# Optimization experiments

Measured on AMD Instinct MI355X. Metric: run time of the kernel, lower is better.

## Reference

```python
import jax, jax.numpy as jnp
import numpy as np

N_QUBITS = 10
N_LAYERS = 4
DIM = 2 ** N_QUBITS  # 1024
IN_FEATURES = 512
OUT_FEATURES = 64
BATCH = 4096


def setup_inputs() -> dict:
    key = jax.random.key(0)
    ks = jax.random.split(key, 6)
    return {
        "x": jax.random.normal(ks[0], (BATCH, IN_FEATURES), dtype=jnp.float32),
        "W_pre": jax.random.normal(ks[1], (DIM, IN_FEATURES), dtype=jnp.float32) / np.float32(np.sqrt(IN_FEATURES)),
        "b_pre": jnp.zeros((DIM,), dtype=jnp.float32),
        "q_weights": jax.random.normal(ks[2], (N_LAYERS, N_QUBITS, 3), dtype=jnp.float32),
        "W_post": jax.random.normal(ks[3], (OUT_FEATURES, N_QUBITS), dtype=jnp.float32) / np.float32(np.sqrt(N_QUBITS)),
        "b_post": jnp.zeros((OUT_FEATURES,), dtype=jnp.float32),
    }


def _rot_matrices(w):
    # w: [L, n, 3] -> PennyLane Rot(phi, theta, omega) = RZ(omega) RY(theta) RZ(phi)
    phi, theta, omega = w[..., 0], w[..., 1], w[..., 2]
    c = jnp.cos(theta / 2).astype(jnp.complex64)
    s = jnp.sin(theta / 2).astype(jnp.complex64)
    e_mm = jnp.exp(-0.5j * (phi + omega))
    e_pp = jnp.exp(0.5j * (phi + omega))
    e_pm = jnp.exp(0.5j * (phi - omega))
    e_mp = jnp.exp(-0.5j * (phi - omega))
    row0 = jnp.stack([e_mm * c, -e_pm * s], axis=-1)
    row1 = jnp.stack([e_mp * s, e_pp * c], axis=-1)
    return jnp.stack([row0, row1], axis=-2)  # [L, n, 2, 2] complex64


def _apply_1q(psi, U, wire):
    # psi: [B, 2, 2, ..., 2]; apply 2x2 unitary U on qubit `wire` (axis wire+1)
    axis = wire + 1
    psi = jnp.moveaxis(psi, axis, -1)
    psi = psi @ U.T  # new[a] = sum_b U[a,b] psi[b]
    return jnp.moveaxis(psi, -1, axis)


def _cnot(psi, control, target):
    ca, ta = control + 1, target + 1
    p0 = jax.lax.index_in_dim(psi, 0, ca, keepdims=True)
    p1 = jax.lax.index_in_dim(psi, 1, ca, keepdims=True)
    p1 = jnp.flip(p1, axis=ta)  # flip target amplitudes where control = 1
    return jnp.concatenate([p0, p1], axis=ca)


def _quantum_forward(amps, q_weights):
    # AmplitudeEmbedding(normalize=True) + StronglyEntanglingLayers + PauliZ expvals, batched.
    B = amps.shape[0]
    norm = jnp.sqrt(jnp.sum(amps * amps, axis=1, keepdims=True))
    psi = (amps / norm).astype(jnp.complex64).reshape((B,) + (2,) * N_QUBITS)
    U = _rot_matrices(q_weights)
    for l in range(N_LAYERS):
        for w in range(N_QUBITS):
            psi = _apply_1q(psi, U[l, w], w)
        r = (l % (N_QUBITS - 1)) + 1  # PennyLane default ranges
        for w in range(N_QUBITS):
            psi = _cnot(psi, w, (w + r) % N_QUBITS)
    probs = psi.real ** 2 + psi.imag ** 2
    axes_all = tuple(range(1, N_QUBITS + 1))
    z = []
    for i in range(N_QUBITS):
        other = tuple(a for a in axes_all if a != i + 1)
        marg = jnp.sum(probs, axis=other)  # [B, 2]
        z.append(marg[:, 0] - marg[:, 1])
    return jnp.stack(z, axis=1)  # [B, n_qubits]


def reference(x, W_pre, b_pre, q_weights, W_post, b_post):
    h = jax.nn.relu(x @ W_pre.T + b_pre)          # [B, 2^n]
    z = _quantum_forward(h, q_weights)            # [B, n_qubits]
    return z @ W_post.T + b_post                  # [B, out_features]
```

## Files before the change

kernel.cpp:

```cpp
#include <hip/hip_runtime.h>
#include <hip/hip_bf16.h>
#include <math.h>

#define NQ   10
#define DIM  1024
#define NL   4
#define INF  512
#define OUTF 64
#define MBATCH 4096

typedef _Float16 half8 __attribute__((ext_vector_type(8)));
typedef float f32x4 __attribute__((ext_vector_type(4)));

#define WS_H16  0
#define WS_X16  (8u * 1024u * 1024u)
#define WS_W16  (12u * 1024u * 1024u)
#define WS_SU   (13u * 1024u * 1024u)

__global__ __launch_bounds__(256) void setup_kernel(
    const float* __restrict__ x, const float* __restrict__ w,
    const float* __restrict__ qw, _Float16* __restrict__ x16,
    _Float16* __restrict__ w16, float* __restrict__ su)
{
    const int bid = blockIdx.x;
    const int tid = threadIdx.x;
    if (bid < 1024) {
        const int base = bid * 2048 + tid * 8;
        float4 a = *reinterpret_cast<const float4*>(x + base);
        float4 b = *reinterpret_cast<const float4*>(x + base + 4);
        half8 o = {(_Float16)a.x, (_Float16)a.y, (_Float16)a.z, (_Float16)a.w,
                   (_Float16)b.x, (_Float16)b.y, (_Float16)b.z, (_Float16)b.w};
        *reinterpret_cast<half8*>(x16 + base) = o;
    } else if (bid < 1280) {
        const int base = (bid - 1024) * 2048 + tid * 8;
        float4 a = *reinterpret_cast<const float4*>(w + base);
        float4 b = *reinterpret_cast<const float4*>(w + base + 4);
        half8 o = {(_Float16)a.x, (_Float16)a.y, (_Float16)a.z, (_Float16)a.w,
                   (_Float16)b.x, (_Float16)b.y, (_Float16)b.z, (_Float16)b.w};
        *reinterpret_cast<half8*>(w16 + base) = o;
    } else {
        if (tid < NL * NQ) {
            float phi = qw[tid * 3 + 0], theta = qw[tid * 3 + 1], omega = qw[tid * 3 + 2];
            float st, ct; sincosf(0.5f * theta, &st, &ct);
            float spm, cpm; sincosf(0.5f * (phi - omega), &spm, &cpm);
            float spp, cpp; sincosf(0.5f * (phi + omega), &spp, &cpp);
            float* o = su + tid * 8;
            o[0] =  cpp * ct; o[1] = -spp * ct;
            o[2] = -cpm * st; o[3] = -spm * st;
            o[4] =  cpm * st; o[5] = -spm * st;
            o[6] =  cpp * ct; o[7] =  spp * ct;
        }
    }
}

__global__ __launch_bounds__(256) void gemm16_kernel(
    const _Float16* __restrict__ X, const _Float16* __restrict__ W,
    const float* __restrict__ bias, _Float16* __restrict__ H)
{
    constexpr int BM = 128, BN = 64, BK = 32, LDP = BK + 8;
    __shared__ _Float16 As[BM][LDP];
    __shared__ _Float16 Bs[BN][LDP];

    const int tid = threadIdx.x;
    const int wave = tid >> 6, lane = tid & 63;
    const int wm = wave >> 1, wn = wave & 1;
    const int l15 = lane & 15, lk = (lane >> 4) * 8;

    const int arow = tid >> 1, ahalf = tid & 1;
    const int brow = tid & 63, bseg = tid >> 6;

    const _Float16* ag = X + (size_t)(blockIdx.x * BM + arow) * INF + ahalf * 16;
    const _Float16* bg = W + (size_t)(blockIdx.y * BN + brow) * INF + bseg * 8;

    f32x4 acc[4][2] = {};

    for (int k0 = 0; k0 < INF; k0 += BK) {
        half8 av0 = *reinterpret_cast<const half8*>(ag + k0);
        half8 av1 = *reinterpret_cast<const half8*>(ag + k0 + 8);
        half8 bv  = *reinterpret_cast<const half8*>(bg + k0);
        __syncthreads();
        *reinterpret_cast<half8*>(&As[arow][ahalf * 16])     = av0;
        *reinterpret_cast<half8*>(&As[arow][ahalf * 16 + 8]) = av1;
        *reinterpret_cast<half8*>(&Bs[brow][bseg * 8])       = bv;
        __syncthreads();
        half8 bfr0 = *reinterpret_cast<const half8*>(&Bs[wn * 32 + l15][lk]);
        half8 bfr1 = *reinterpret_cast<const half8*>(&Bs[wn * 32 + 16 + l15][lk]);
#pragma unroll
        for (int mi = 0; mi < 4; ++mi) {
            half8 afr = *reinterpret_cast<const half8*>(&As[wm * 64 + mi * 16 + l15][lk]);
            acc[mi][0] = __builtin_amdgcn_mfma_f32_16x16x32_f16(afr, bfr0, acc[mi][0], 0, 0, 0);
            acc[mi][1] = __builtin_amdgcn_mfma_f32_16x16x32_f16(afr, bfr1, acc[mi][1], 0, 0, 0);
        }
    }

    const int crow0 = blockIdx.x * BM + wm * 64;
    const int ccol0 = blockIdx.y * BN + wn * 32;
#pragma unroll
    for (int ni = 0; ni < 2; ++ni) {
        const int col = ccol0 + ni * 16 + l15;
        const float bb = bias[col];
#pragma unroll
        for (int mi = 0; mi < 4; ++mi) {
#pragma unroll
            for (int r = 0; r < 4; ++r) {
                const int row = crow0 + mi * 16 + (lane >> 4) * 4 + r;
                const float o = fmaxf(acc[mi][ni][r] + bb, 0.f);
                H[(size_t)row * DIM + col] = (_Float16)o;
            }
        }
    }
}

template<int ML>
__device__ __forceinline__ float lxor(float v, int bpa) {
    if constexpr (ML == 32)
        return __int_as_float(__builtin_amdgcn_ds_bpermute(bpa, __float_as_int(v)));
    else if constexpr (ML == 16)
        return __int_as_float(__builtin_amdgcn_ds_swizzle(__float_as_int(v), 0x401F));
    else if constexpr (ML == 8)
        return __int_as_float(__builtin_amdgcn_mov_dpp(__float_as_int(v), 0x128, 0xF, 0xF, false));
    else if constexpr (ML == 4)
        return __int_as_float(__builtin_amdgcn_ds_swizzle(__float_as_int(v), 0x101F));
    else if constexpr (ML == 2)
        return __int_as_float(__builtin_amdgcn_mov_dpp(__float_as_int(v), 0x4E, 0xF, 0xF, false));
    else
        return __int_as_float(__builtin_amdgcn_mov_dpp(__float_as_int(v), 0xB1, 0xF, 0xF, false));
}

__device__ __forceinline__ int perm_chain(int j, int r) {
#pragma unroll
    for (int w2 = NQ - 1; w2 >= 0; --w2) {
        const int cb = 9 - w2;
        const int tb = 9 - ((w2 + r) % NQ);
        j ^= ((j >> cb) & 1) << tb;
    }
    return j;
}

template<int W>
__device__ __forceinline__ void lane_gate(float re[16], float im[16],
                                          const float* up, int lane, int bpa) {
    constexpr int ML = 1 << (5 - W);
    const float4 ua = *reinterpret_cast<const float4*>(up + W * 8);
    const float4 ub = *reinterpret_cast<const float4*>(up + W * 8 + 4);
    const bool hi = (lane & ML) != 0;
    const float cmr = hi ? ub.z : ua.x;
    const float cmi = hi ? ub.w : ua.y;
    const float cpr = hi ? ub.x : ua.z;
    const float cpi = hi ? ub.y : ua.w;
#pragma unroll
    for (int k = 0; k < 16; ++k) {
        const float pr = lxor<ML>(re[k], bpa);
        const float pi = lxor<ML>(im[k], bpa);
        const float ar = re[k], ai = im[k];
        re[k] = cmr * ar - cmi * ai + cpr * pr - cpi * pi;
        im[k] = cmr * ai + cmi * ar + cpr * pi + cpi * pr;
    }
}

__global__ __launch_bounds__(64) void quantum_kernel(
    const _Float16* __restrict__ Hbuf, const float* __restrict__ sug,
    const float* __restrict__ W_post, const float* __restrict__ b_post,
    float* __restrict__ out)
{
    __shared__ float sre[DIM];
    __shared__ float sim[DIM];

    const int lane = threadIdx.x;
    const int b = blockIdx.x;
    const int bpa = (lane ^ 32) << 2;

    const _Float16* hr = Hbuf + (size_t)b * DIM + (lane << 4);
    float re[16], im[16];
    {
        half8 h0 = *reinterpret_cast<const half8*>(hr);
        half8 h1 = *reinterpret_cast<const half8*>(hr + 8);
#pragma unroll
        for (int j = 0; j < 8; ++j) { re[j] = (float)h0[j]; re[8 + j] = (float)h1[j]; }
    }
    float nrm = 0.f;
#pragma unroll
    for (int k = 0; k < 16; ++k) nrm = fmaf(re[k], re[k], nrm);
#pragma unroll
    for (int m = 1; m < 64; m <<= 1) nrm += __shfl_xor(nrm, m, 64);
    const float rn = rsqrtf(nrm);
#pragma unroll
    for (int k = 0; k < 16; ++k) { re[k] *= rn; im[k] = 0.f; }

    for (int l = 0; l < NL; ++l) {
        const float* up = sug + l * NQ * 8;

        lane_gate<0>(re, im, up, lane, bpa);
        lane_gate<1>(re, im, up, lane, bpa);
        lane_gate<2>(re, im, up, lane, bpa);
        lane_gate<3>(re, im, up, lane, bpa);
        lane_gate<4>(re, im, up, lane, bpa);
        lane_gate<5>(re, im, up, lane, bpa);

#pragma unroll
        for (int w = 6; w < 10; ++w) {
            const int mk = 1 << (9 - w);
            const float4 ua = *reinterpret_cast<const float4*>(up + w * 8);
            const float4 ub = *reinterpret_cast<const float4*>(up + w * 8 + 4);
#pragma unroll
            for (int k = 0; k < 16; ++k) {
                if (!(k & mk)) {
                    const int k1 = k | mk;
                    const float a0r = re[k], a0i = im[k];
                    const float a1r = re[k1], a1i = im[k1];
                    re[k]  = ua.x * a0r - ua.y * a0i + ua.z * a1r - ua.w * a1i;
                    im[k]  = ua.x * a0i + ua.y * a0r + ua.z * a1i + ua.w * a1r;
                    re[k1] = ub.x * a0r - ub.y * a0i + ub.z * a1r - ub.w * a1i;
                    im[k1] = ub.x * a0i + ub.y * a0r + ub.z * a1i + ub.w * a1r;
                }
            }
        }

        const int r = l + 1;
        const int jbase = perm_chain(lane << 4, r);
        const int c0 = perm_chain(1, r);
        const int c1 = perm_chain(2, r);
        const int c2 = perm_chain(4, r);
        const int c3 = perm_chain(8, r);
        const int m = (lane >> 1) & 15;
        const int wbase = lane << 4;
        __syncthreads();
#pragma unroll
        for (int k = 0; k < 16; ++k) {
            sre[wbase | (k ^ m)] = re[k];
            sim[wbase | (k ^ m)] = im[k];
        }
        __syncthreads();
#pragma unroll
        for (int k = 0; k < 16; ++k) {
            int jk = 0;
            if (k & 1) jk ^= c0;
            if (k & 2) jk ^= c1;
            if (k & 4) jk ^= c2;
            if (k & 8) jk ^= c3;
            const int j = jbase ^ jk;
            const int slot = (j & ~15) | ((j & 15) ^ ((j >> 5) & 15));
            re[k] = sre[slot];
            im[k] = sim[slot];
        }
    }

    float ptot = 0.f, zk0 = 0.f, zk1 = 0.f, zk2 = 0.f, zk3 = 0.f;
#pragma unroll
    for (int k = 0; k < 16; ++k) {
        const float p = re[k] * re[k] + im[k] * im[k];
        ptot += p;
        zk0 += (k & 8) ? -p : p;
        zk1 += (k & 4) ? -p : p;
        zk2 += (k & 2) ? -p : p;
        zk3 += (k & 1) ? -p : p;
    }
    float z[NQ];
#pragma unroll
    for (int w = 0; w < 6; ++w)
        z[w] = ((lane >> (5 - w)) & 1) ? -ptot : ptot;
    z[6] = zk0; z[7] = zk1; z[8] = zk2; z[9] = zk3;
#pragma unroll
    for (int w = 0; w < NQ; ++w)
#pragma unroll
        for (int m2 = 1; m2 < 64; m2 <<= 1)
            z[w] += __shfl_xor(z[w], m2, 64);

    float o = b_post[lane];
#pragma unroll
    for (int w = 0; w < NQ; ++w)
        o = fmaf(z[w], W_post[lane * NQ + w], o);
    out[(size_t)b * OUTF + lane] = o;
}

extern "C" void kernel_launch(void* const* d_in, const int* in_sizes, int n_in,
                              void* d_out, int out_size, void* d_ws, size_t ws_size,
                              hipStream_t stream) {
    const float* x      = (const float*)d_in[0];
    const float* W_pre  = (const float*)d_in[1];
    const float* b_pre  = (const float*)d_in[2];
    const float* qw     = (const float*)d_in[3];
    const float* W_post = (const float*)d_in[4];
    const float* b_post = (const float*)d_in[5];
    float* out = (float*)d_out;

    char* ws = (char*)d_ws;
    _Float16* h16 = (_Float16*)(ws + WS_H16);
    _Float16* x16 = (_Float16*)(ws + WS_X16);
    _Float16* w16 = (_Float16*)(ws + WS_W16);
    float*    su  = (float*)   (ws + WS_SU);

    setup_kernel<<<1281, 256, 0, stream>>>(x, W_pre, qw, x16, w16, su);
    dim3 g1(MBATCH / 128, DIM / 64);
    gemm16_kernel<<<g1, 256, 0, stream>>>(x16, w16, b_pre, h16);
    quantum_kernel<<<MBATCH, 64, 0, stream>>>(h16, su, W_post, b_post, out);
}
```

Before: 64.92 us.

## Fold CNOT permutations into gate index masks, removing LDS shuffles in quantum kernel

```diff
diff --git a/kernel.cpp b/kernel.cpp
--- a/kernel.cpp
+++ b/kernel.cpp
@@ -11,11 +11,57 @@
 
 typedef _Float16 half8 __attribute__((ext_vector_type(8)));
 typedef float f32x4 __attribute__((ext_vector_type(4)));
+typedef float f32x2 __attribute__((ext_vector_type(2)));
 
 #define WS_H16  0
 #define WS_X16  (8u * 1024u * 1024u)
 #define WS_W16  (12u * 1024u * 1024u)
 #define WS_SU   (13u * 1024u * 1024u)
+
+constexpr int fstep(int j, int r) {
+    for (int w2 = NQ - 1; w2 >= 0; --w2) {
+        const int cb = 9 - w2;
+        const int tb = 9 - ((w2 + r) % NQ);
+        j ^= ((j >> cb) & 1) << tb;
+    }
+    return j;
+}
+constexpr int ifstep(int j, int r) {
+    for (int w2 = 0; w2 < NQ; ++w2) {
+        const int cb = 9 - w2;
+        const int tb = 9 - ((w2 + r) % NQ);
+        j ^= ((j >> cb) & 1) << tb;
+    }
+    return j;
+}
+constexpr int sigma_fwd(int l, int x) {
+    for (int t = l - 1; t >= 0; --t) x = fstep(x, t + 1);
+    return x;
+}
+constexpr int sigma_inv(int l, int s) {
+    for (int t = 0; t < l; ++t) s = ifstep(s, t + 1);
+    return s;
+}
+constexpr int gate_m(int l, int b) { return sigma_fwd(l, 1 << b); }
+constexpr int gate_g(int l, int b) {
+    int g = 0;
+    for (int j = 0; j < NQ; ++j)
+        if ((sigma_inv(l, 1 << j) >> b) & 1) g |= 1 << j;
+    return g;
+}
+struct QM { int v[NQ]; };
+constexpr QM make_qm() {
+    QM q{};
+    for (int w = 0; w < NQ; ++w) {
+        const int B = 9 - w;
+        int m = 0;
+        for (int j = 0; j < NQ; ++j)
+            if ((sigma_inv(NL, 1 << j) >> B) & 1) m |= 1 << j;
+        q.v[w] = m;
+    }
+    return q;
+}
+constexpr QM QMASKS = make_qm();
 
 __global__ __launch_bounds__(256) void setup_kernel(
     const float* __restrict__ x, const float* __restrict__ w,
@@ -111,166 +157,148 @@
     }
 }
 
-template<int ML>
-__device__ __forceinline__ float lxor(float v, int bpa) {
-    if constexpr (ML == 32)
-        return __int_as_float(__builtin_amdgcn_ds_bpermute(bpa, __float_as_int(v)));
-    else if constexpr (ML == 16)
-        return __int_as_float(__builtin_amdgcn_ds_swizzle(__float_as_int(v), 0x401F));
-    else if constexpr (ML == 8)
+template<int MHI>
+__device__ __forceinline__ float lx(float v, int lane) {
+    if constexpr (MHI == 0)
+        return v;
+    else if constexpr (MHI == 1)
+        return __int_as_float(__builtin_amdgcn_mov_dpp(__float_as_int(v), 0xB1, 0xF, 0xF, false));
+    else if constexpr (MHI == 2)
+        return __int_as_float(__builtin_amdgcn_mov_dpp(__float_as_int(v), 0x4E, 0xF, 0xF, false));
+    else if constexpr (MHI == 3)
+        return __int_as_float(__builtin_amdgcn_mov_dpp(__float_as_int(v), 0x1B, 0xF, 0xF, false));
+    else if constexpr (MHI == 8)
         return __int_as_float(__builtin_amdgcn_mov_dpp(__float_as_int(v), 0x128, 0xF, 0xF, false));
-    else if constexpr (ML == 4)
-        return __int_as_float(__builtin_amdgcn_ds_swizzle(__float_as_int(v), 0x101F));
-    else if constexpr (ML == 2)
-        return __int_as_float(__builtin_amdgcn_mov_dpp(__float_as_int(v), 0x4E, 0xF, 0xF, false));
+    else if constexpr (MHI < 32)
+        return __int_as_float(__builtin_amdgcn_ds_swizzle(__float_as_int(v), 0x1F | (MHI << 10)));
     else
-        return __int_as_float(__builtin_amdgcn_mov_dpp(__float_as_int(v), 0xB1, 0xF, 0xF, false));
-}
-
-__device__ __forceinline__ int perm_chain(int j, int r) {
-#pragma unroll
-    for (int w2 = NQ - 1; w2 >= 0; --w2) {
-        const int cb = 9 - w2;
-        const int tb = 9 - ((w2 + r) % NQ);
-        j ^= ((j >> cb) & 1) << tb;
-    }
-    return j;
-}
-
-template<int W>
-__device__ __forceinline__ void lane_gate(float re[16], float im[16],
-                                          const float* up, int lane, int bpa) {
-    constexpr int ML = 1 << (5 - W);
-    const float4 ua = *reinterpret_cast<const float4*>(up + W * 8);
-    const float4 ub = *reinterpret_cast<const float4*>(up + W * 8 + 4);
-    const bool hi = (lane & ML) != 0;
-    const float cmr = hi ? ub.z : ua.x;
-    const float cmi = hi ? ub.w : ua.y;
-    const float cpr = hi ? ub.x : ua.z;
-    const float cpi = hi ? ub.y : ua.w;
+        return __int_as_float(__builtin_amdgcn_ds_bpermute((lane ^ MHI) << 2, __float_as_int(v)));
+}
+
+template<int L, int W>
+__device__ __forceinline__ void apply_gate(f32x2 rr[8], f32x2 ii[8],
+                                           const float* __restrict__ su, int lane)
+{
+    constexpr int b   = 9 - W;
+    constexpr int m   = gate_m(L, b);
+    constexpr int g   = gate_g(L, b);
+    constexpr int MHI = m >> 4, MLO = m & 15;
+    constexpr int GHI = g >> 4, GLO = g & 15;
+
+    const float4 ua = *reinterpret_cast<const float4*>(su + (L * NQ + W) * 8);
+    const float4 ub = *reinterpret_cast<const float4*>(su + (L * NQ + W) * 8 + 4);
+    const bool hl = __builtin_popcount(lane & GHI) & 1;
+
+    const float cmr0 = hl ? ub.z : ua.x, cmi0 = hl ? ub.w : ua.y;
+    const float cpr0 = hl ? ub.x : ua.z, cpi0 = hl ? ub.y : ua.w;
+    const float cmr1 = hl ? ua.x : ub.z, cmi1 = hl ? ua.y : ub.w;
+    const float cpr1 = hl ? ua.z : ub.x, cpi1 = hl ? ua.w : ub.y;
+
+    float pr[16], pi[16];
 #pragma unroll
     for (int k = 0; k < 16; ++k) {
-        const float pr = lxor<ML>(re[k], bpa);
-        const float pi = lxor<ML>(im[k], bpa);
-        const float ar = re[k], ai = im[k];
-        re[k] = cmr * ar - cmi * ai + cpr * pr - cpi * pi;
-        im[k] = cmr * ai + cmi * ar + cpr * pi + cpi * pr;
-    }
-}
-
-__global__ __launch_bounds__(64) void quantum_kernel(
+        const int kp = k ^ MLO;
+        const float vr = (kp & 1) ? rr[kp >> 1].y : rr[kp >> 1].x;
+        const float vi = (kp & 1) ? ii[kp >> 1].y : ii[kp >> 1].x;
+        pr[k] = lx<MHI>(vr, lane);
+        pi[k] = lx<MHI>(vi, lane);
+    }
+#pragma unroll
+    for (int j = 0; j < 8; ++j) {
+        const int k0 = 2 * j, k1 = 2 * j + 1;
+        const int h0 = __builtin_popcount(k0 & GLO) & 1;
+        const int h1 = __builtin_popcount(k1 & GLO) & 1;
+        f32x2 CMR, CMI, CPR, CPI, PR, PI;
+        CMR.x = h0 ? cmr1 : cmr0;  CMR.y = h1 ? cmr1 : cmr0;
+        CMI.x = h0 ? cmi1 : cmi0;  CMI.y = h1 ? cmi1 : cmi0;
+        CPR.x = h0 ? cpr1 : cpr0;  CPR.y = h1 ? cpr1 : cpr0;
+        CPI.x = h0 ? cpi1 : cpi0;  CPI.y = h1 ? cpi1 : cpi0;
+        PR.x = pr[k0]; PR.y = pr[k1];
+        PI.x = pi[k0]; PI.y = pi[k1];
+        const f32x2 R = rr[j], I = ii[j];
+        rr[j] = R * CMR - I * CMI + PR * CPR - PI * CPI;
+        ii[j] = I * CMR + R * CMI + PI * CPR + PR * CPI;
+    }
+}
+
+template<int L>
+__device__ __forceinline__ void apply_layer(f32x2 rr[8], f32x2 ii[8],
+                                            const float* __restrict__ su, int lane)
+{
+    apply_gate<L, 0>(rr, ii, su, lane);
+    apply_gate<L, 1>(rr, ii, su, lane);
+    apply_gate<L, 2>(rr, ii, su, lane);
+    apply_gate<L, 3>(rr, ii, su, lane);
+    apply_gate<L, 4>(rr, ii, su, lane);
+    apply_gate<L, 5>(rr, ii, su, lane);
+    apply_gate<L, 6>(rr, ii, su, lane);
+    apply_gate<L, 7>(rr, ii, su, lane);
+    apply_gate<L, 8>(rr, ii, su, lane);
+    apply_gate<L, 9>(rr, ii, su, lane);
+}
+
+__global__ __launch_bounds__(256) void quantum_kernel(
     const _Float16* __restrict__ Hbuf, const float* __restrict__ sug,
     const float* __restrict__ W_post, const float* __restrict__ b_post,
     float* __restrict__ out)
 {
-    __shared__ float sre[DIM];
-    __shared__ float sim[DIM];
-
     const int lane = threadIdx.x;
-    const int b = blockIdx.x;
-    const int bpa = (lane ^ 32) << 2;
-
-    const _Float16* hr = Hbuf + (size_t)b * DIM + (lane << 4);
-    float re[16], im[16];
+    const int row  = blockIdx.x * 4 + threadIdx.y;
+
+    const _Float16* hr = Hbuf + (size_t)row * DIM + (lane << 4);
+    f32x2 rr[8], ii[8];
     {
         half8 h0 = *reinterpret_cast<const half8*>(hr);
         half8 h1 = *reinterpret_cast<const half8*>(hr + 8);
 #pragma unroll
-        for (int j = 0; j < 8; ++j) { re[j] = (float)h0[j]; re[8 + j] = (float)h1[j]; }
-    }
-    float nrm = 0.f;
-#pragma unroll
-    for (int k = 0; k < 16; ++k) nrm = fmaf(re[k], re[k], nrm);
-#pragma unroll
-    for (int m = 1; m < 64; m <<= 1) nrm += __shfl_xor(nrm, m, 64);
-    const float rn = rsqrtf(nrm);
-#pragma unroll
-    for (int k = 0; k < 16; ++k) { re[k] *= rn; im[k] = 0.f; }
-
-    for (int l = 0; l < NL; ++l) {
-        const float* up = sug + l * NQ * 8;
-
-        lane_gate<0>(re, im, up, lane, bpa);
-        lane_gate<1>(re, im, up, lane, bpa);
-        lane_gate<2>(re, im, up, lane, bpa);
-        lane_gate<3>(re, im, up, lane, bpa);
-        lane_gate<4>(re, im, up, lane, bpa);
-        lane_gate<5>(re, im, up, lane, bpa);
-
-#pragma unroll
-        for (int w = 6; w < 10; ++w) {
-            const int mk = 1 << (9 - w);
-            const float4 ua = *reinterpret_cast<const float4*>(up + w * 8);
-            const float4 ub = *reinterpret_cast<const float4*>(up + w * 8 + 4);
-#pragma unroll
-            for (int k = 0; k < 16; ++k) {
-                if (!(k & mk)) {
-                    const int k1 = k | mk;
-                    const float a0r = re[k], a0i = im[k];
-                    const float a1r = re[k1], a1i = im[k1];
-                    re[k]  = ua.x * a0r - ua.y * a0i + ua.z * a1r - ua.w * a1i;
-                    im[k]  = ua.x * a0i + ua.y * a0r + ua.z * a1i + ua.w * a1r;
-                    re[k1] = ub.x * a0r - ub.y * a0i + ub.z * a1r - ub.w * a1i;
-                    im[k1] = ub.x * a0i + ub.y * a0r + ub.z * a1i + ub.w * a1r;
-                }
-            }
-        }
-
-        const int r = l + 1;
-        const int jbase = perm_chain(lane << 4, r);
-        const int c0 = perm_chain(1, r);
-        const int c1 = perm_chain(2, r);
-        const int c2 = perm_chain(4, r);
-        const int c3 = perm_chain(8, r);
-        const int m = (lane >> 1) & 15;
-        const int wbase = lane << 4;
-        __syncthreads();
-#pragma unroll
-        for (int k = 0; k < 16; ++k) {
-            sre[wbase | (k ^ m)] = re[k];
-            sim[wbase | (k ^ m)] = im[k];
-        }
-        __syncthreads();
-#pragma unroll
-        for (int k = 0; k < 16; ++k) {
-            int jk = 0;
-            if (k & 1) jk ^= c0;
-            if (k & 2) jk ^= c1;
-            if (k & 4) jk ^= c2;
-            if (k & 8) jk ^= c3;
-            const int j = jbase ^ jk;
-            const int slot = (j & ~15) | ((j & 15) ^ ((j >> 5) & 15));
-            re[k] = sre[slot];
-            im[k] = sim[slot];
-        }
-    }
-
-    float ptot = 0.f, zk0 = 0.f, zk1 = 0.f, zk2 = 0.f, zk3 = 0.f;
-#pragma unroll
-    for (int k = 0; k < 16; ++k) {
-        const float p = re[k] * re[k] + im[k] * im[k];
-        ptot += p;
-        zk0 += (k & 8) ? -p : p;
-        zk1 += (k & 4) ? -p : p;
-        zk2 += (k & 2) ? -p : p;
-        zk3 += (k & 1) ? -p : p;
-    }
+        for (int j = 0; j < 4; ++j) {
+            rr[j].x     = (float)h0[2 * j];     rr[j].y     = (float)h0[2 * j + 1];
+            rr[j + 4].x = (float)h1[2 * j];     rr[j + 4].y = (float)h1[2 * j + 1];
+            ii[j]     = f32x2{0.f, 0.f};
+            ii[j + 4] = f32x2{0.f, 0.f};
+        }
+    }
+    f32x2 n2 = f32x2{0.f, 0.f};
+#pragma unroll
+    for (int j = 0; j < 8; ++j) n2 += rr[j] * rr[j];
+    float nrm = n2.x + n2.y;
+#pragma unroll
+    for (int m2 = 1; m2 < 64; m2 <<= 1) nrm += __shfl_xor(nrm, m2, 64);
+    const float inv_nrm = 1.0f / nrm;
+
+    apply_layer<0>(rr, ii, sug, lane);
+    apply_layer<1>(rr, ii, sug, lane);
+    apply_layer<2>(rr, ii, sug, lane);
+    apply_layer<3>(rr, ii, sug, lane);
+
+    f32x2 P[8];
+#pragma unroll
+    for (int j = 0; j < 8; ++j) P[j] = rr[j] * rr[j] + ii[j] * ii[j];
+
     float z[NQ];
 #pragma unroll
-    for (int w = 0; w < 6; ++w)
-        z[w] = ((lane >> (5 - w)) & 1) ? -ptot : ptot;
-    z[6] = zk0; z[7] = zk1; z[8] = zk2; z[9] = zk3;
-#pragma unroll
-    for (int w = 0; w < NQ; ++w)
-#pragma unroll
-        for (int m2 = 1; m2 < 64; m2 <<= 1)
-            z[w] += __shfl_xor(z[w], m2, 64);
+    for (int w = 0; w < NQ; ++w) {
+        const int q = QMASKS.v[w];
+        const int qhi = q >> 4, qlo = q & 15;
+        float zl = 0.f;
+#pragma unroll
+        for (int j = 0; j < 8; ++j) {
+            const float s0 = (__builtin_popcount((2 * j) & qlo) & 1) ? -1.f : 1.f;
+            const float s1 = (__builtin_popcount((2 * j + 1) & qlo) & 1) ? -1.f : 1.f;
+            zl += s0 * P[j].x;
+            zl += s1 * P[j].y;
+        }
+        if (__builtin_popcount(lane & qhi) & 1) zl = -zl;
+#pragma unroll
+        for (int m2 = 1; m2 < 64; m2 <<= 1) zl += __shfl_xor(zl, m2, 64);
+        z[w] = zl * inv_nrm;
+    }
 
     float o = b_post[lane];
 #pragma unroll
     for (int w = 0; w < NQ; ++w)
         o = fmaf(z[w], W_post[lane * NQ + w], o);
-    out[(size_t)b * OUTF + lane] = o;
+    out[(size_t)row * OUTF + lane] = o;
 }
 
 extern "C" void kernel_launch(void* const* d_in, const int* in_sizes, int n_in,
@@ -293,5 +321,5 @@
     setup_kernel<<<1281, 256, 0, stream>>>(x, W_pre, qw, x16, w16, su);
     dim3 g1(MBATCH / 128, DIM / 64);
     gemm16_kernel<<<g1, 256, 0, stream>>>(x16, w16, b_pre, h16);
-    quantum_kernel<<<MBATCH, 64, 0, stream>>>(h16, su, W_post, b_post, out);
-}
+    quantum_kernel<<<MBATCH / 4, dim3(64, 4), 0, stream>>>(h16, su, W_post, b_post, out);
+}
```

New measurement: 62.26 us. 1.04x faster.
